# Kernel optimization log

Hardware: AMD Instinct MI355X
Metric: run time of the kernel (lower is better)

Reference implementation:

```python
import jax, jax.numpy as jnp
import numpy as np

NEG_SLOPE = 0.2
EPS = 1e-16


def gat_conv(x, edge_index, W, a_src, a_dst, b, num_nodes):
    """PyG-style GATConv: heads inferred from a_src.shape[0], concat=True.
    x: [N, F_in], W: [F_in, H*C], a_src/a_dst: [H, C], b: [H*C].
    Adds self-loops, computes per-edge attention with leaky_relu,
    segment softmax over incoming edges per destination, scatter-add aggregate.
    """
    H, C = a_src.shape
    loops = jnp.arange(num_nodes, dtype=edge_index.dtype)
    src = jnp.concatenate([edge_index[0], loops])
    dst = jnp.concatenate([edge_index[1], loops])

    h = (x @ W).reshape(num_nodes, H, C)            # [N, H, C]
    alpha_s = jnp.einsum('nhc,hc->nh', h, a_src)    # [N, H]
    alpha_d = jnp.einsum('nhc,hc->nh', h, a_dst)    # [N, H]

    e = alpha_s[src] + alpha_d[dst]                 # [E, H]
    e = jax.nn.leaky_relu(e, NEG_SLOPE)

    # segment softmax over edges grouped by destination node
    m = jax.ops.segment_max(e, dst, num_segments=num_nodes)   # [N, H]
    ex = jnp.exp(e - m[dst])
    s = jax.ops.segment_sum(ex, dst, num_segments=num_nodes)  # [N, H]
    alpha = ex / (s[dst] + EPS)                     # [E, H]

    msg = h[src] * alpha[..., None]                 # [E, H, C]
    out = jax.ops.segment_sum(msg, dst, num_segments=num_nodes)  # [N, H, C]
    return out.reshape(num_nodes, H * C) + b


def setup_inputs() -> dict:
    key = jax.random.key(0)
    ks = jax.random.split(key, 12)
    N, E = 50000, 800000
    input_dim, hidden_dim, latent_dim, heads = 128, 32, 32, 8

    x = jax.random.normal(ks[0], (N, input_dim), dtype=jnp.float32)
    edge_index = jax.random.randint(ks[1], (2, E), 0, N, dtype=jnp.int64)

    def glorot(k, shape):
        fan = shape[0] + shape[-1]
        return jax.random.normal(k, shape, dtype=jnp.float32) * jnp.sqrt(2.0 / fan)

    W1 = glorot(ks[2], (input_dim, heads * hidden_dim))
    a_src1 = glorot(ks[3], (heads, hidden_dim))
    a_dst1 = glorot(ks[4], (heads, hidden_dim))
    b1 = jnp.zeros((heads * hidden_dim,), dtype=jnp.float32)

    W2 = glorot(ks[5], (heads * hidden_dim, latent_dim))
    a_src2 = glorot(ks[6], (1, latent_dim))
    a_dst2 = glorot(ks[7], (1, latent_dim))
    b2 = jnp.zeros((latent_dim,), dtype=jnp.float32)

    Wd = glorot(ks[8], (latent_dim, input_dim))
    bd = jnp.zeros((input_dim,), dtype=jnp.float32)

    return {"x": x, "edge_index": edge_index,
            "W1": W1, "a_src1": a_src1, "a_dst1": a_dst1, "b1": b1,
            "W2": W2, "a_src2": a_src2, "a_dst2": a_dst2, "b2": b2,
            "Wd": Wd, "bd": bd}


def reference(x, edge_index, W1, a_src1, a_dst1, b1, W2, a_src2, a_dst2, b2, Wd, bd):
    N = x.shape[0]
    h = jax.nn.relu(gat_conv(x, edge_index, W1, a_src1, a_dst1, b1, N))
    z = gat_conv(h, edge_index, W2, a_src2, a_dst2, b2, N)
    return z @ Wd + bd
```

## Files before the change

kernel.cpp:

```cpp
#include <hip/hip_runtime.h>
#include <math.h>

#define NEG_SLOPE 0.2f

typedef float f32x4_t __attribute__((ext_vector_type(4)));

static __device__ __forceinline__ float leaky(float x) {
  return x > 0.0f ? x : NEG_SLOPE * x;
}

static __device__ __forceinline__ void nt_store4(float* p, float a, float b, float c, float d) {
  f32x4_t v = {a, b, c, d};
  __builtin_nontemporal_store(v, (f32x4_t*)p);
}

static __device__ __forceinline__ unsigned short f32_to_bf16(float f) {
  unsigned int u = __float_as_uint(f);
  unsigned int r = u + 0x7FFFu + ((u >> 16) & 1u);
  return (unsigned short)(r >> 16);
}
static __device__ __forceinline__ float bf16_to_f32(unsigned short h) {
  return __uint_as_float(((unsigned int)h) << 16);
}

__global__ void zero_kernel(int* __restrict__ p, int n) {
  int i = blockIdx.x * blockDim.x + threadIdx.x;
  if (i < n) p[i] = 0;
}

__global__ void count_kernel(const int* __restrict__ ei, int* __restrict__ counts, int E) {
  int i = blockIdx.x * blockDim.x + threadIdx.x;
  if (i < E) atomicAdd(&counts[ei[E + i]], 1);
}

__global__ void scan_kernel(const int* __restrict__ counts, int* __restrict__ offs,
                            int* __restrict__ cursor, int N) {
  __shared__ int sums[1024];
  int tid = threadIdx.x;
  int chunk = (N + 1023) >> 10;
  int start = tid * chunk;
  int end = min(start + chunk, N);
  int s = 0;
  for (int i = start; i < end; ++i) s += counts[i];
  sums[tid] = s;
  __syncthreads();
  for (int off = 1; off < 1024; off <<= 1) {
    int v = (tid >= off) ? sums[tid - off] : 0;
    __syncthreads();
    sums[tid] += v;
    __syncthreads();
  }
  int run = (tid > 0) ? sums[tid - 1] : 0;
  for (int i = start; i < end; ++i) {
    offs[i] = run;
    cursor[i] = run;
    run += counts[i];
  }
  if (tid == 0) offs[N] = sums[1023];
}

__global__ void fill_kernel(const int* __restrict__ ei, int* __restrict__ cursor,
                            int* __restrict__ csr, int E) {
  int i = blockIdx.x * blockDim.x + threadIdx.x;
  if (i < E) {
    int src = ei[i];
    int dst = ei[E + i];
    int pos = atomicAdd(&cursor[dst], 1);
    csr[pos] = src;
  }
}

template <bool BIAS>
__global__ __launch_bounds__(256) void gemm_tiled(const float* __restrict__ A,
                                                  const float* __restrict__ B,
                                                  const float* __restrict__ bias,
                                                  float* __restrict__ C,
                                                  int M, int N, int K) {
  __shared__ float As[16][68];
  __shared__ float Bs[16][68];
  int tid = threadIdx.x;
  int tx = tid & 15, ty = tid >> 4;
  int brow = blockIdx.x * 64, bcol = blockIdx.y * 64;

  float acc[4][4] = {};

  int arow = tid >> 2;
  int akv = (tid & 3) * 4;
  int bkk = tid >> 4;
  int bcv = (tid & 15) * 4;

  for (int k0 = 0; k0 < K; k0 += 16) {
    int gr = min(brow + arow, M - 1);
    float4 av = *(const float4*)&A[(size_t)gr * K + k0 + akv];
    float4 bv;
    int gc = bcol + bcv;
    if (gc + 3 < N)
      bv = *(const float4*)&B[(size_t)(k0 + bkk) * N + gc];
    else
      bv = make_float4(0.f, 0.f, 0.f, 0.f);

    __syncthreads();
    As[akv + 0][arow] = av.x;
    As[akv + 1][arow] = av.y;
    As[akv + 2][arow] = av.z;
    As[akv + 3][arow] = av.w;
    *(float4*)&Bs[bkk][bcv] = bv;
    __syncthreads();

#pragma unroll
    for (int kk = 0; kk < 16; ++kk) {
      float4 a4 = *(const float4*)&As[kk][ty * 4];
      float4 b4 = *(const float4*)&Bs[kk][tx * 4];
      float ar[4] = {a4.x, a4.y, a4.z, a4.w};
      float br[4] = {b4.x, b4.y, b4.z, b4.w};
#pragma unroll
      for (int i = 0; i < 4; ++i)
#pragma unroll
        for (int j = 0; j < 4; ++j) acc[i][j] = fmaf(ar[i], br[j], acc[i][j]);
    }
  }

#pragma unroll
  for (int i = 0; i < 4; ++i) {
    int r = brow + ty * 4 + i;
    if (r >= M) continue;
#pragma unroll
    for (int j = 0; j < 4; ++j) {
      int c = bcol + tx * 4 + j;
      if (c >= N) continue;
      float v = acc[i][j];
      if (BIAS) v += bias[c];
      C[(size_t)r * N + c] = v;
    }
  }
}

template <bool BIAS, bool OUT_BF16>
__global__ __launch_bounds__(256) void gemm_big(const float* __restrict__ A,
                                                const float* __restrict__ B,
                                                const float* __restrict__ bias,
                                                float* __restrict__ C,
                                                unsigned short* __restrict__ C16,
                                                int M, int N, int K) {
  __shared__ float As[16][128];
  __shared__ float Bs[16][128];
  int tid = threadIdx.x;
  int tx = tid & 15, ty = tid >> 4;
  int brow = blockIdx.y * 128, bcol = blockIdx.x * 128;

  float acc[8][8] = {};

  int ar = tid >> 1;
  int akv = (tid & 1) * 8;
  int bk = tid >> 4;
  int bcv = (tid & 15) * 8;

  const float* Aptr = A + (size_t)min(brow + ar, M - 1) * K + akv;
  const float* Bptr = B + (size_t)bk * N + bcol + bcv;

  for (int k0 = 0; k0 < K; k0 += 16) {
    float4 a0 = *(const float4*)(Aptr + k0);
    float4 a1 = *(const float4*)(Aptr + k0 + 4);
    float4 b0 = *(const float4*)(Bptr + (size_t)k0 * N);
    float4 b1 = *(const float4*)(Bptr + (size_t)k0 * N + 4);

    __syncthreads();
    As[akv + 0][ar] = a0.x;
    As[akv + 1][ar] = a0.y;
    As[akv + 2][ar] = a0.z;
    As[akv + 3][ar] = a0.w;
    As[akv + 4][ar] = a1.x;
    As[akv + 5][ar] = a1.y;
    As[akv + 6][ar] = a1.z;
    As[akv + 7][ar] = a1.w;
    *(float4*)&Bs[bk][bcv] = b0;
    *(float4*)&Bs[bk][bcv + 4] = b1;
    __syncthreads();

#pragma unroll
    for (int kk = 0; kk < 16; ++kk) {
      float4 av0 = *(const float4*)&As[kk][ty * 8];
      float4 av1 = *(const float4*)&As[kk][ty * 8 + 4];
      float4 bv0 = *(const float4*)&Bs[kk][tx * 8];
      float4 bv1 = *(const float4*)&Bs[kk][tx * 8 + 4];
      float ar8[8] = {av0.x, av0.y, av0.z, av0.w, av1.x, av1.y, av1.z, av1.w};
      float br8[8] = {bv0.x, bv0.y, bv0.z, bv0.w, bv1.x, bv1.y, bv1.z, bv1.w};
#pragma unroll
      for (int i = 0; i < 8; ++i)
#pragma unroll
        for (int j = 0; j < 8; ++j) acc[i][j] = fmaf(ar8[i], br8[j], acc[i][j]);
    }
  }

#pragma unroll
  for (int i = 0; i < 8; ++i) {
    int r = brow + ty * 8 + i;
    if (r >= M) continue;
    if (OUT_BF16) {
      int c = bcol + tx * 8;
      ushort4 v0, v1;
      v0.x = f32_to_bf16(acc[i][0]);
      v0.y = f32_to_bf16(acc[i][1]);
      v0.z = f32_to_bf16(acc[i][2]);
      v0.w = f32_to_bf16(acc[i][3]);
      v1.x = f32_to_bf16(acc[i][4]);
      v1.y = f32_to_bf16(acc[i][5]);
      v1.z = f32_to_bf16(acc[i][6]);
      v1.w = f32_to_bf16(acc[i][7]);
      *(ushort4*)&C16[(size_t)r * N + c] = v0;
      *(ushort4*)&C16[(size_t)r * N + c + 4] = v1;
    } else {
#pragma unroll
      for (int j0 = 0; j0 < 8; j0 += 4) {
        int c = bcol + tx * 8 + j0;
        float4 v = {acc[i][j0], acc[i][j0 + 1], acc[i][j0 + 2], acc[i][j0 + 3]};
        if (BIAS) {
          float4 bb = *(const float4*)&bias[c];
          v.x += bb.x; v.y += bb.y; v.z += bb.z; v.w += bb.w;
        }
        *(float4*)&C[(size_t)r * N + c] = v;
      }
    }
  }
}

__global__ __launch_bounds__(256) void alpha1_kernel(const unsigned short* __restrict__ h1b,
                                                     const float* __restrict__ a_src,
                                                     const float* __restrict__ a_dst,
                                                     float* __restrict__ as_out,
                                                     float* __restrict__ ad_out, int N) {
  int wid = (int)((blockIdx.x * (size_t)blockDim.x + threadIdx.x) >> 6);
  int lane = threadIdx.x & 63;
  if (wid >= N) return;
  ushort4 hq = *(const ushort4*)&h1b[(size_t)wid * 256 + lane * 4];
  float4 sv = *(const float4*)&a_src[lane * 4];
  float4 dv = *(const float4*)&a_dst[lane * 4];
  float hx = bf16_to_f32(hq.x), hy = bf16_to_f32(hq.y);
  float hz = bf16_to_f32(hq.z), hw = bf16_to_f32(hq.w);
  float ps = hx * sv.x + hy * sv.y + hz * sv.z + hw * sv.w;
  float pd = hx * dv.x + hy * dv.y + hz * dv.z + hw * dv.w;
  ps += __shfl_xor(ps, 1); ps += __shfl_xor(ps, 2); ps += __shfl_xor(ps, 4);
  pd += __shfl_xor(pd, 1); pd += __shfl_xor(pd, 2); pd += __shfl_xor(pd, 4);
  if ((lane & 7) == 0) {
    as_out[wid * 8 + (lane >> 3)] = ps;
    ad_out[wid * 8 + (lane >> 3)] = pd;
  }
}

__global__ __launch_bounds__(256) void agg1_kernel(const int* __restrict__ offs,
                                                   const int* __restrict__ csr,
                                                   const unsigned short* __restrict__ h1b,
                                                   const float* __restrict__ as1,
                                                   const float* __restrict__ ad1,
                                                   const float* __restrict__ b1,
                                                   float* __restrict__ h2, int N) {
  int wid = (int)((blockIdx.x * (size_t)blockDim.x + threadIdx.x) >> 6);
  int lane = threadIdx.x & 63;
  if (wid >= N) return;
  int head = lane >> 3;

  float ad = ad1[wid * 8 + head];
  float p0 = __expf(fminf(leaky(as1[wid * 8 + head] + ad), 80.0f));
  float s = p0;
  ushort4 hq0 = *(const ushort4*)&h1b[(size_t)wid * 256 + lane * 4];
  float4 acc;
  acc.x = p0 * bf16_to_f32(hq0.x);
  acc.y = p0 * bf16_to_f32(hq0.y);
  acc.z = p0 * bf16_to_f32(hq0.z);
  acc.w = p0 * bf16_to_f32(hq0.w);

  auto step = [&](float a0, const ushort4& hv) {
    float p = __expf(fminf(leaky(a0 + ad), 80.0f));
    s += p;
    acc.x = fmaf(p, bf16_to_f32(hv.x), acc.x);
    acc.y = fmaf(p, bf16_to_f32(hv.y), acc.y);
    acc.z = fmaf(p, bf16_to_f32(hv.z), acc.z);
    acc.w = fmaf(p, bf16_to_f32(hv.w), acc.w);
  };

  int j0 = offs[wid], j1 = offs[wid + 1];
  int j = j0;
  for (; j + 8 <= j1; j += 8) {
    int si[8];
    float a[8];
    ushort4 hv[8];
#pragma unroll
    for (int u = 0; u < 8; ++u) si[u] = csr[j + u];
#pragma unroll
    for (int u = 0; u < 8; ++u) a[u] = as1[si[u] * 8 + head];
#pragma unroll
    for (int u = 0; u < 8; ++u) hv[u] = *(const ushort4*)&h1b[(size_t)si[u] * 256 + lane * 4];
#pragma unroll
    for (int u = 0; u < 8; ++u) step(a[u], hv[u]);
  }
  for (; j + 4 <= j1; j += 4) {
    int si[4];
    float a[4];
    ushort4 hv[4];
#pragma unroll
    for (int u = 0; u < 4; ++u) si[u] = csr[j + u];
#pragma unroll
    for (int u = 0; u < 4; ++u) a[u] = as1[si[u] * 8 + head];
#pragma unroll
    for (int u = 0; u < 4; ++u) hv[u] = *(const ushort4*)&h1b[(size_t)si[u] * 256 + lane * 4];
#pragma unroll
    for (int u = 0; u < 4; ++u) step(a[u], hv[u]);
  }
  for (; j < j1; ++j) {
    int s0 = csr[j];
    float a0 = as1[s0 * 8 + head];
    ushort4 h0 = *(const ushort4*)&h1b[(size_t)s0 * 256 + lane * 4];
    step(a0, h0);
  }

  float rs = 1.0f / (s + 1e-16f);
  float4 bv = *(const float4*)&b1[lane * 4];
  nt_store4(&h2[(size_t)wid * 256 + lane * 4],
            fmaxf(fmaf(acc.x, rs, bv.x), 0.0f),
            fmaxf(fmaf(acc.y, rs, bv.y), 0.0f),
            fmaxf(fmaf(acc.z, rs, bv.z), 0.0f),
            fmaxf(fmaf(acc.w, rs, bv.w), 0.0f));
}

__global__ __launch_bounds__(256) void alpha2_kernel(const float* __restrict__ hl2,
                                                     const float* __restrict__ a_src,
                                                     const float* __restrict__ a_dst,
                                                     float* __restrict__ as2,
                                                     float* __restrict__ ad2, int N) {
  int wid = (int)((blockIdx.x * (size_t)blockDim.x + threadIdx.x) >> 6);
  int lane = threadIdx.x & 63;
  if (wid >= N) return;
  int c = lane & 31;
  float w = (lane < 32) ? a_src[c] : a_dst[c];
  float v = hl2[(size_t)wid * 32 + c];
  float p = v * w;
  p += __shfl_xor(p, 1); p += __shfl_xor(p, 2); p += __shfl_xor(p, 4);
  p += __shfl_xor(p, 8); p += __shfl_xor(p, 16);
  if (lane == 0) as2[wid] = p;
  if (lane == 32) ad2[wid] = p;
}

__global__ __launch_bounds__(256) void agg2_kernel(const int* __restrict__ offs,
                                                   const int* __restrict__ csr,
                                                   const float* __restrict__ hl2,
                                                   const float* __restrict__ as2,
                                                   const float* __restrict__ ad2,
                                                   const float* __restrict__ b2,
                                                   float* __restrict__ z, int N) {
  int wid = (int)((blockIdx.x * (size_t)blockDim.x + threadIdx.x) >> 6);
  int lane = threadIdx.x & 63;
  if (wid >= N) return;
  int c = lane & 31;

  float ad = ad2[wid];
  float p0 = __expf(fminf(leaky(as2[wid] + ad), 80.0f));
  float s = p0;
  float acc = p0 * hl2[(size_t)wid * 32 + c];

  auto step = [&](float a0, float v0) {
    float p = __expf(fminf(leaky(a0 + ad), 80.0f));
    s += p;
    acc = fmaf(p, v0, acc);
  };

  int j0 = offs[wid], j1 = offs[wid + 1];
  int j = j0;
  for (; j + 8 <= j1; j += 8) {
    int si[8];
    float a[8], v[8];
#pragma unroll
    for (int u = 0; u < 8; ++u) si[u] = csr[j + u];
#pragma unroll
    for (int u = 0; u < 8; ++u) a[u] = as2[si[u]];
#pragma unroll
    for (int u = 0; u < 8; ++u) v[u] = hl2[(size_t)si[u] * 32 + c];
#pragma unroll
    for (int u = 0; u < 8; ++u) step(a[u], v[u]);
  }
  for (; j < j1; ++j) {
    int s0 = csr[j];
    step(as2[s0], hl2[(size_t)s0 * 32 + c]);
  }

  if (lane < 32) {
    float rs = 1.0f / (s + 1e-16f);
    z[(size_t)wid * 32 + c] = fmaf(acc, rs, b2[c]);
  }
}

extern "C" void kernel_launch(void* const* d_in, const int* in_sizes, int n_in,
                              void* d_out, int out_size, void* d_ws, size_t ws_size,
                              hipStream_t stream) {
  const float* x = (const float*)d_in[0];
  const int* ei = (const int*)d_in[1];
  const float* W1 = (const float*)d_in[2];
  const float* a_src1 = (const float*)d_in[3];
  const float* a_dst1 = (const float*)d_in[4];
  const float* b1 = (const float*)d_in[5];
  const float* W2 = (const float*)d_in[6];
  const float* a_src2 = (const float*)d_in[7];
  const float* a_dst2 = (const float*)d_in[8];
  const float* b2 = (const float*)d_in[9];
  const float* Wd = (const float*)d_in[10];
  const float* bd = (const float*)d_in[11];
  float* out = (float*)d_out;

  const int IN = 128, HC1 = 256, C2 = 32, OUT = 128;
  int N = in_sizes[0] / IN;
  int E = in_sizes[1] / 2;

  char* p = (char*)d_ws;
  auto alloc = [&](size_t bytes) {
    void* r = (void*)p;
    p += (bytes + 255) & ~(size_t)255;
    return r;
  };
  unsigned short* h1b = (unsigned short*)alloc((size_t)N * HC1 * 2);
  float* as1 = (float*)alloc((size_t)N * 8 * 4);
  float* ad1 = (float*)alloc((size_t)N * 8 * 4);
  float* h2 = (float*)alloc((size_t)N * HC1 * 4);
  float* hl2 = (float*)alloc((size_t)N * C2 * 4);
  float* as2 = (float*)alloc((size_t)N * 4);
  float* ad2 = (float*)alloc((size_t)N * 4);
  float* z = (float*)alloc((size_t)N * C2 * 4);
  int* counts = (int*)alloc((size_t)N * 4);
  int* cursor = (int*)alloc((size_t)N * 4);
  int* offs = (int*)alloc((size_t)(N + 1) * 4);
  int* csr = (int*)alloc((size_t)E * 4);

  int nblk = (N + 255) / 256;
  int eblk = (E + 255) / 256;
  int wblk = (int)(((size_t)N * 64 + 255) / 256);

  zero_kernel<<<nblk, 256, 0, stream>>>(counts, N);
  count_kernel<<<eblk, 256, 0, stream>>>(ei, counts, E);
  scan_kernel<<<1, 1024, 0, stream>>>(counts, offs, cursor, N);
  fill_kernel<<<eblk, 256, 0, stream>>>(ei, cursor, csr, E);

  {
    dim3 g(HC1 / 128, (N + 127) / 128);
    gemm_big<false, true><<<g, 256, 0, stream>>>(x, W1, nullptr, nullptr, h1b, N, HC1, IN);
  }
  alpha1_kernel<<<wblk, 256, 0, stream>>>(h1b, a_src1, a_dst1, as1, ad1, N);
  agg1_kernel<<<wblk, 256, 0, stream>>>(offs, csr, h1b, as1, ad1, b1, h2, N);

  {
    dim3 g((N + 63) / 64, 1);
    gemm_tiled<false><<<g, 256, 0, stream>>>(h2, W2, nullptr, hl2, N, C2, HC1);
  }
  alpha2_kernel<<<wblk, 256, 0, stream>>>(hl2, a_src2, a_dst2, as2, ad2, N);
  agg2_kernel<<<wblk, 256, 0, stream>>>(offs, csr, hl2, as2, ad2, b2, z, N);

  {
    dim3 g(OUT / 128, (N + 127) / 128);
    gemm_big<true, false><<<g, 256, 0, stream>>>(z, Wd, bd, out, nullptr, N, OUT, C2);
  }
}
```

Baseline: 496.2 us.

## Replace single-block CSR offset scan with multi-block three-phase scan

The exclusive prefix sum over per-node in-degree counts ran in one 1024-thread block, with each thread walking a contiguous chunk serially. It is now split into three kernels: per-block partial sums, a single-block scan of the block sums, and a per-block scan that writes offsets and cursors using vectorized loads. This spreads the scan across many CUs and makes the memory accesses coalesced, at the cost of two extra kernel launches. It assumes at most 1024 scan blocks.

```diff
diff --git a/kernel.cpp b/kernel.cpp
--- a/kernel.cpp
+++ b/kernel.cpp
@@ -33,30 +33,72 @@
   if (i < E) atomicAdd(&counts[ei[E + i]], 1);
 }
 
-__global__ void scan_kernel(const int* __restrict__ counts, int* __restrict__ offs,
-                            int* __restrict__ cursor, int N) {
-  __shared__ int sums[1024];
+__global__ __launch_bounds__(256) void partial_kernel(const int* __restrict__ counts,
+                                                      int* __restrict__ bsums, int N) {
+  __shared__ int red[256];
+  int b = blockIdx.x, tid = threadIdx.x;
+  int base = b * 1024;
+  int s = 0;
+  for (int i = tid; i < 1024; i += 256) {
+    int idx = base + i;
+    if (idx < N) s += counts[idx];
+  }
+  red[tid] = s;
+  __syncthreads();
+  for (int off = 128; off > 0; off >>= 1) {
+    if (tid < off) red[tid] += red[tid + off];
+    __syncthreads();
+  }
+  if (tid == 0) bsums[b] = red[0];
+}
+
+__global__ __launch_bounds__(1024) void scanb_kernel(const int* __restrict__ bsums,
+                                                     int* __restrict__ boffs,
+                                                     int* __restrict__ offs, int N, int nb) {
+  __shared__ int sh[1024];
   int tid = threadIdx.x;
-  int chunk = (N + 1023) >> 10;
-  int start = tid * chunk;
-  int end = min(start + chunk, N);
-  int s = 0;
-  for (int i = start; i < end; ++i) s += counts[i];
-  sums[tid] = s;
+  sh[tid] = (tid < nb) ? bsums[tid] : 0;
   __syncthreads();
   for (int off = 1; off < 1024; off <<= 1) {
-    int v = (tid >= off) ? sums[tid - off] : 0;
-    __syncthreads();
-    sums[tid] += v;
-    __syncthreads();
-  }
-  int run = (tid > 0) ? sums[tid - 1] : 0;
-  for (int i = start; i < end; ++i) {
-    offs[i] = run;
-    cursor[i] = run;
-    run += counts[i];
-  }
-  if (tid == 0) offs[N] = sums[1023];
+    int v = (tid >= off) ? sh[tid - off] : 0;
+    __syncthreads();
+    sh[tid] += v;
+    __syncthreads();
+  }
+  if (tid < nb) boffs[tid] = (tid > 0) ? sh[tid - 1] : 0;
+  if (tid == 0) offs[N] = sh[1023];
+}
+
+__global__ __launch_bounds__(256) void scanc_kernel(const int* __restrict__ counts,
+                                                    const int* __restrict__ boffs,
+                                                    int* __restrict__ offs,
+                                                    int* __restrict__ cursor, int N) {
+  __shared__ int sh[256];
+  int b = blockIdx.x, tid = threadIdx.x;
+  int base = b * 1024 + tid * 4;
+  int c0 = 0, c1 = 0, c2 = 0, c3 = 0;
+  if (base + 3 < N) {
+    int4 v = *(const int4*)&counts[base];
+    c0 = v.x; c1 = v.y; c2 = v.z; c3 = v.w;
+  } else {
+    if (base + 0 < N) c0 = counts[base + 0];
+    if (base + 1 < N) c1 = counts[base + 1];
+    if (base + 2 < N) c2 = counts[base + 2];
+  }
+  int tsum = c0 + c1 + c2 + c3;
+  sh[tid] = tsum;
+  __syncthreads();
+  for (int off = 1; off < 256; off <<= 1) {
+    int v = (tid >= off) ? sh[tid - off] : 0;
+    __syncthreads();
+    sh[tid] += v;
+    __syncthreads();
+  }
+  int run = boffs[b] + sh[tid] - tsum;
+  if (base + 0 < N) { offs[base + 0] = run; cursor[base + 0] = run; run += c0; }
+  if (base + 1 < N) { offs[base + 1] = run; cursor[base + 1] = run; run += c1; }
+  if (base + 2 < N) { offs[base + 2] = run; cursor[base + 2] = run; run += c2; }
+  if (base + 3 < N) { offs[base + 3] = run; cursor[base + 3] = run; }
 }
 
 __global__ void fill_kernel(const int* __restrict__ ei, int* __restrict__ cursor,
@@ -427,6 +469,9 @@
   int* cursor = (int*)alloc((size_t)N * 4);
   int* offs = (int*)alloc((size_t)(N + 1) * 4);
   int* csr = (int*)alloc((size_t)E * 4);
+  int nscan = (N + 1023) / 1024;
+  int* bsums = (int*)alloc((size_t)nscan * 4);
+  int* boffs = (int*)alloc((size_t)nscan * 4);
 
   int nblk = (N + 255) / 256;
   int eblk = (E + 255) / 256;
@@ -434,7 +479,9 @@
 
   zero_kernel<<<nblk, 256, 0, stream>>>(counts, N);
   count_kernel<<<eblk, 256, 0, stream>>>(ei, counts, E);
-  scan_kernel<<<1, 1024, 0, stream>>>(counts, offs, cursor, N);
+  partial_kernel<<<nscan, 256, 0, stream>>>(counts, bsums, N);
+  scanb_kernel<<<1, 1024, 0, stream>>>(bsums, boffs, offs, N, nscan);
+  scanc_kernel<<<nscan, 256, 0, stream>>>(counts, boffs, offs, cursor, N);
   fill_kernel<<<eblk, 256, 0, stream>>>(ei, cursor, csr, E);
 
   {
```

After: 402.3 us. -18.9%, faster.
